# Performance work log

Hardware: AMD Instinct MI355X
Metric: run time of the kernel (lower is better)

Reference implementation:

```python
import jax, jax.numpy as jnp
import numpy as np

N_Q, N_X, N_Z = 1024, 512, 512
N_PER = N_Q + N_X + N_Z        # 2048 nodes per graph
B = 16                          # graphs per batch
DEG = 16                        # avg in/out degree
E_PER = N_PER * DEG
N = B * N_PER                   # 32768 total nodes
E = B * E_PER                   # 524288 total edges
HID, HEADS, L = 128, 4, 3
DH = HID // HEADS               # 32 per-head dim
EPS = 1e-5


def setup_inputs() -> dict:
    key = jax.random.key(0)
    ks = jax.random.split(key, 10)
    # one-hot node-type features (qubit / X-stab / Z-stab), tiled over batch
    sn = jnp.zeros((N_PER, 3), jnp.float32)
    sn = sn.at[:N_Q, 0].set(1.0).at[N_Q:N_Q + N_X, 1].set(1.0).at[N_Q + N_X:, 2].set(1.0)
    x = jnp.tile(sn, (B, 1))  # [N,3]
    # random sparse edges, graph-local then offset (mimics dense_to_sparse + Batch)
    src = jax.random.randint(ks[0], (B, E_PER), 0, N_PER)
    dst = jax.random.randint(ks[1], (B, E_PER), 0, N_PER)
    off = (jnp.arange(B) * N_PER)[:, None]
    edge_src = (src + off).reshape(-1).astype(jnp.int32)
    edge_dst = (dst + off).reshape(-1).astype(jnp.int32)
    seg = jnp.repeat(jnp.arange(B, dtype=jnp.int32), N_PER)  # graph id per node
    s = 0.05
    return dict(
        x=x, edge_src=edge_src, edge_dst=edge_dst, seg=seg,
        in_w=jax.random.normal(ks[2], (3, HID)) * s, in_b=jnp.zeros((HID,)),
        qw=jax.random.normal(ks[3], (L, HID, HID)) * s, qb=jnp.zeros((L, HID)),
        kw=jax.random.normal(ks[4], (L, HID, HID)) * s, kb=jnp.zeros((L, HID)),
        vw=jax.random.normal(ks[5], (L, HID, HID)) * s, vb=jnp.zeros((L, HID)),
        sw=jax.random.normal(ks[6], (L, HID, HID)) * s, sb=jnp.zeros((L, HID)),
        fw=jax.random.normal(ks[7], (L, HID, HID)) * s, fb=jnp.zeros((L, HID)),
        ln_g=jnp.ones((L, HID)), ln_b=jnp.zeros((L, HID)),
    )


def _layer_norm(h, g, b):
    mu = jnp.mean(h, axis=-1, keepdims=True)
    var = jnp.mean(jnp.square(h - mu), axis=-1, keepdims=True)
    return (h - mu) * jax.lax.rsqrt(var + EPS) * g + b


def reference(x, edge_src, edge_dst, seg, in_w, in_b, qw, qb, kw, kb, vw, vb,
              sw, sb, fw, fb, ln_g, ln_b):
    scale = 1.0 / jnp.sqrt(jnp.float32(DH))
    h = x @ in_w + in_b  # [N,HID]
    for i in range(L):
        h_res = h
        # TransformerConv: per-edge multi-head attention (softmax over in-neighbors)
        q = (h @ qw[i] + qb[i]).reshape(N, HEADS, DH)
        k = (h @ kw[i] + kb[i]).reshape(N, HEADS, DH)
        v = (h @ vw[i] + vb[i]).reshape(N, HEADS, DH)
        logits = jnp.einsum('ehd,ehd->eh', q[edge_dst], k[edge_src]) * scale  # [E,H]
        m = jax.ops.segment_max(logits, edge_dst, num_segments=N)             # [N,H]
        e = jnp.exp(logits - m[edge_dst])
        z = jax.ops.segment_sum(e, edge_dst, num_segments=N)                  # [N,H]
        alpha = e / z[edge_dst]
        agg = jax.ops.segment_sum(alpha[:, :, None] * v[edge_src], edge_dst,
                                  num_segments=N).reshape(N, HID)
        h = agg + h @ sw[i] + sb[i]        # root/skip linear (root_weight=True)
        # dropout is a no-op in eval mode
        h = h + jax.nn.relu(h @ fw[i] + fb[i])   # FFN residual
        h = h + h_res                            # outer residual
        h = jax.nn.relu(_layer_norm(h, ln_g[i], ln_b[i]))
    # global_mean_pool over graphs
    tot = jax.ops.segment_sum(h, seg, num_segments=B)                       # [B,HID]
    cnt = jax.ops.segment_sum(jnp.ones((N, 1), h.dtype), seg, num_segments=B)
    return tot / cnt
```

## Files before the change

### kernel.cpp

```cpp
#include <hip/hip_runtime.h>
#include <hip/hip_bf16.h>

#define N_TOT 32768
#define E_TOT 524288
#define HID 128
#define B_GR 16
#define NPER 2048
#define LAYERS 3
#define EPSLN 1e-5f
#define ELLW 64
#define SCALE_L2E (0.17677669529663687f * 1.4426950408889634f)

typedef float f4 __attribute__((ext_vector_type(4)));
typedef short bf16x8 __attribute__((ext_vector_type(8)));
typedef unsigned short u16x4 __attribute__((ext_vector_type(4)));

__device__ __forceinline__ unsigned short f2bf_rne(float x) {
    unsigned u = __float_as_uint(x);
    unsigned r = (u + 0x7FFFu + ((u >> 16) & 1u)) >> 16;
    return (unsigned short)r;
}

__device__ __forceinline__ float bf2f(unsigned short u) {
    return __uint_as_float(((unsigned)u) << 16);
}

__device__ __forceinline__ void unpack8(uint4 w, float* f) {
    f[0] = __uint_as_float(w.x << 16); f[1] = __uint_as_float(w.x & 0xFFFF0000u);
    f[2] = __uint_as_float(w.y << 16); f[3] = __uint_as_float(w.y & 0xFFFF0000u);
    f[4] = __uint_as_float(w.z << 16); f[5] = __uint_as_float(w.z & 0xFFFF0000u);
    f[6] = __uint_as_float(w.w << 16); f[7] = __uint_as_float(w.w & 0xFFFF0000u);
}

__global__ __launch_bounds__(256) void k_zp(const float* __restrict__ qw, const float* __restrict__ kw,
                                            const float* __restrict__ vw, const float* __restrict__ sw,
                                            const float* __restrict__ fw, unsigned short* __restrict__ wt,
                                            int* __restrict__ cursor, float* __restrict__ outz) {
    if (blockIdx.x < 960) {
        int mid = blockIdx.x >> 6;
        int within = (blockIdx.x & 63) * 256 + threadIdx.x;
        int l = mid / 5, t = mid % 5;
        const float* src = (t == 0 ? qw : t == 1 ? kw : t == 2 ? vw : t == 3 ? sw : fw) + l * HID * HID;
        int c = within >> 7;
        int kk = within & 127;
        int k = kk ^ ((c & 7) << 3);
        float sc = (t == 0) ? SCALE_L2E : 1.0f;
        wt[mid * HID * HID + c * HID + kk] = f2bf_rne(src[k * HID + c] * sc);
    } else if (blockIdx.x < 992) {
        int i = (blockIdx.x - 960) * 256 + threadIdx.x;
        reinterpret_cast<int4*>(cursor)[i] = int4{0, 0, 0, 0};
    } else {
        f4 z4 = {0.f, 0.f, 0.f, 0.f};
        reinterpret_cast<f4*>(outz)[threadIdx.x * 2] = z4;
        reinterpret_cast<f4*>(outz)[threadIdx.x * 2 + 1] = z4;
    }
}

#define GEMM_COMPUTE(acc, AL)                                                               \
    {                                                                                       \
        _Pragma("unroll")                                                                   \
        for (int ks = 0; ks < 4; ++ks) {                                                    \
            bf16x8 a0 = *reinterpret_cast<const bf16x8*>(                                   \
                &AL[wm * 32 + lr][(ks * 32 + lg * 8) ^ swz]);                               \
            bf16x8 a1 = *reinterpret_cast<const bf16x8*>(                                   \
                &AL[wm * 32 + 16 + lr][(ks * 32 + lg * 8) ^ swz]);                          \
            _Pragma("unroll")                                                               \
            for (int n = 0; n < 4; ++n) {                                                   \
                bf16x8 b = *reinterpret_cast<const bf16x8*>(                                \
                    &W_lds[wn * 64 + n * 16 + lr][(ks * 32 + lg * 8) ^ swz]);               \
                acc[0][n] = __builtin_amdgcn_mfma_f32_16x16x32_bf16(a0, b, acc[0][n], 0, 0, 0); \
                acc[1][n] = __builtin_amdgcn_mfma_f32_16x16x32_bf16(a1, b, acc[1][n], 0, 0, 0); \
            }                                                                               \
        }                                                                                   \
    }

#define ZERO_ACC(acc)                                                        \
    {                                                                        \
        _Pragma("unroll")                                                    \
        for (int m = 0; m < 2; ++m)                                          \
            _Pragma("unroll")                                                \
            for (int n = 0; n < 4; ++n) acc[m][n] = f4{0, 0, 0, 0};          \
    }

#define COPY_W(SRC)                                                          \
    {                                                                        \
        _Pragma("unroll")                                                    \
        for (int p = 0; p < 8; ++p)                                          \
            reinterpret_cast<uint4*>(&W_lds[0][0])[p * 256 + tid] =          \
                reinterpret_cast<const uint4*>(SRC)[p * 256 + tid];          \
    }

#define QKV_EPILOGUE(ACC, T_IDX)                                                            \
    {                                                                                       \
        _Pragma("unroll")                                                                   \
        for (int n = 0; n < 4; ++n) {                                                       \
            int col = wn * 64 + n * 16 + lr;                                                \
            float bs = biases[T_IDX][col];                                                  \
            if (T_IDX == 0) bs *= SCALE_L2E;                                                \
            unsigned short* outp = (T_IDX == 0) ? oq : okv + ((T_IDX == 2) ? 128 : 0);      \
            const size_t stride = (T_IDX == 0) ? HID : 256;                                 \
            _Pragma("unroll")                                                               \
            for (int m = 0; m < 2; ++m) {                                                   \
                _Pragma("unroll")                                                           \
                for (int r = 0; r < 4; ++r) {                                               \
                    int row = r0 + wm * 32 + m * 16 + lg * 4 + r;                           \
                    outp[(size_t)row * stride + col] = f2bf_rne(ACC[m][n][r] + bs);         \
                }                                                                           \
            }                                                                               \
        }                                                                                   \
    }

__global__ __launch_bounds__(256) void k_scatter_init(const int* __restrict__ esrc, const int* __restrict__ edst,
                                                      int* __restrict__ cursor, unsigned short* __restrict__ ell,
                                                      const float* __restrict__ x,
                                                      const float* __restrict__ in_w,
                                                      const float* __restrict__ in_b,
                                                      const unsigned short* __restrict__ wl,
                                                      const float* __restrict__ qb, const float* __restrict__ kb,
                                                      const float* __restrict__ vb,
                                                      unsigned short* __restrict__ h16,
                                                      unsigned short* __restrict__ oq,
                                                      unsigned short* __restrict__ okv) {
    __shared__ unsigned short A_lds[64][HID];
    __shared__ unsigned short W_lds[HID][HID];
    int tid = threadIdx.x;
    if (blockIdx.x < E_TOT / 256) {
        int e = blockIdx.x * 256 + tid;
        int d = edst[e];
        int pos = atomicAdd(&cursor[d], 1);
        if (pos < ELLW) ell[d * ELLW + pos] = (unsigned short)esrc[e];
        return;
    }
    int r0 = (blockIdx.x - E_TOT / 256) * 64;
    int lane = tid & 63, w = tid >> 6;
    int wm = w >> 1, wn = w & 1;
    int lr = lane & 15, lg = lane >> 4;
    int swz = (lane & 7) << 3;

    #pragma unroll
    for (int p = 0; p < 8; ++p) {
        int idx = p * 256 + tid;
        int row = idx >> 5;
        int k0 = (idx & 31) * 4;
        int n = r0 + row;
        float x0 = x[n * 3 + 0], x1 = x[n * 3 + 1], x2 = x[n * 3 + 2];
        u16x4 b;
        #pragma unroll
        for (int i = 0; i < 4; ++i) {
            int c = k0 + i;
            b[i] = f2bf_rne(x0 * in_w[c] + x1 * in_w[HID + c] + x2 * in_w[2 * HID + c] + in_b[c]);
        }
        int cs = k0 ^ ((row & 7) << 3);
        *reinterpret_cast<u16x4*>(&A_lds[row][cs]) = b;
        *reinterpret_cast<u16x4*>(&h16[(size_t)n * HID + cs]) = b;
    }

    const float* biases[3] = {qb, kb, vb};
    f4 acc[2][4];
    #pragma unroll
    for (int t = 0; t < 3; ++t) {
        COPY_W(wl + t * HID * HID);
        __syncthreads();
        ZERO_ACC(acc);
        GEMM_COMPUTE(acc, A_lds);
        QKV_EPILOGUE(acc, t);
        __syncthreads();
    }
}

__global__ __launch_bounds__(256) void k_attn5(const unsigned short* __restrict__ qb16,
                                               const unsigned short* __restrict__ kv16,
                                               const int* __restrict__ deg,
                                               const unsigned short* __restrict__ ell,
                                               unsigned short* __restrict__ outagg) {
    int bid = blockIdx.x;
    int xcd = bid & 7;
    int chunk = bid >> 3;
    int g2 = xcd + 8 * (chunk >> 9);
    int nb = g2 * 512 + (chunk & 511);
    int n = nb * 4 + (threadIdx.x >> 6);

    int lane = threadIdx.x & 63;
    int g = lane >> 4, l = lane & 15;
    int dg = deg[n];
    if (dg > ELLW) dg = ELLW;
    const unsigned short* eb = ell + n * ELLW;

    float qf[8];
    {
        uint4 qw = *reinterpret_cast<const uint4*>(&qb16[(size_t)n * HID + l * 8]);
        unpack8(qw, qf);
    }

    float z = 0.f;
    float a[8] = {0, 0, 0, 0, 0, 0, 0, 0};
    int nit = (dg + 3) >> 2;
    if (nit > 0) {
        int j = g;
        bool val = j < dg;
        int sj = val ? (int)eb[j] : 0;
        const unsigned short* kv = kv16 + (size_t)sj * 256 + l * 8;
        uint4 kw = *reinterpret_cast<const uint4*>(kv);
        uint4 vw = *reinterpret_cast<const uint4*>(kv + 128);
        for (int it = 0; it < nit; ++it) {
            int jn = j + 4;
            bool valn = jn < dg;
            int sn = valn ? (int)eb[jn] : 0;
            const unsigned short* kvn = kv16 + (size_t)sn * 256 + l * 8;
            uint4 kwn = *reinterpret_cast<const uint4*>(kvn);
            uint4 vwn = *reinterpret_cast<const uint4*>(kvn + 128);
            float kf[8]; unpack8(kw, kf);
            float d = qf[0] * kf[0] + qf[1] * kf[1] + qf[2] * kf[2] + qf[3] * kf[3] +
                      qf[4] * kf[4] + qf[5] * kf[5] + qf[6] * kf[6] + qf[7] * kf[7];
            d += __shfl_xor(d, 1);
            d += __shfl_xor(d, 2);
            float p = val ? exp2f(d) : 0.f;
            z += p;
            float vf[8]; unpack8(vw, vf);
            #pragma unroll
            for (int c = 0; c < 8; ++c) a[c] += p * vf[c];
            kw = kwn; vw = vwn; j = jn; val = valn;
        }
    }
    #pragma unroll
    for (int off = 16; off <= 32; off <<= 1) {
        z += __shfl_xor(z, off);
        #pragma unroll
        for (int c = 0; c < 8; ++c) a[c] += __shfl_xor(a[c], off);
    }
    if (g == 0) {
        float inv = (z > 0.f) ? 1.f / z : 0.f;
        uint4 o;
        o.x = (unsigned)f2bf_rne(a[0] * inv) | ((unsigned)f2bf_rne(a[1] * inv) << 16);
        o.y = (unsigned)f2bf_rne(a[2] * inv) | ((unsigned)f2bf_rne(a[3] * inv) << 16);
        o.z = (unsigned)f2bf_rne(a[4] * inv) | ((unsigned)f2bf_rne(a[5] * inv) << 16);
        o.w = (unsigned)f2bf_rne(a[6] * inv) | ((unsigned)f2bf_rne(a[7] * inv) << 16);
        *reinterpret_cast<uint4*>(&outagg[(size_t)n * HID + l * 8]) = o;
    }
}

template <bool QKV>
__global__ __launch_bounds__(256) void k_fused(const unsigned short* __restrict__ h16,
                                               const unsigned short* __restrict__ wsf,
                                               const float* __restrict__ sb,
                                               const float* __restrict__ fb,
                                               const unsigned short* __restrict__ agg16,
                                               const float* __restrict__ gma,
                                               const float* __restrict__ beta,
                                               unsigned short* __restrict__ out16,
                                               const unsigned short* __restrict__ wqkv,
                                               const float* __restrict__ qb2,
                                               const float* __restrict__ kb2,
                                               const float* __restrict__ vb2,
                                               unsigned short* __restrict__ oq,
                                               unsigned short* __restrict__ okv,
                                               float* __restrict__ pool_out) {
    __shared__ __align__(16) char smem[50432];
    unsigned short (*A_lds)[HID] = reinterpret_cast<unsigned short (*)[HID]>(smem);
    unsigned short (*W_lds)[HID] = reinterpret_cast<unsigned short (*)[HID]>(smem + 16384);
    float (*T)[133] = reinterpret_cast<float (*)[133]>(smem + 16384);

    int tid = threadIdx.x;
    int r0 = blockIdx.x * 64;
    int lane = tid & 63, w = tid >> 6;
    int wm = w >> 1, wn = w & 1;
    int lr = lane & 15, lg = lane >> 4;
    int swz = (lane & 7) << 3;

    {
        const uint4* hs = reinterpret_cast<const uint4*>(h16 + (size_t)r0 * HID);
        #pragma unroll
        for (int p = 0; p < 4; ++p)
            reinterpret_cast<uint4*>(&A_lds[0][0])[p * 256 + tid] = hs[p * 256 + tid];
    }
    COPY_W(wsf);
    __syncthreads();
    f4 acc[2][4];
    ZERO_ACC(acc);
    GEMM_COMPUTE(acc, A_lds);
    __syncthreads();

    unsigned short hres[2][4][4];
    #pragma unroll
    for (int n = 0; n < 4; ++n) {
        int col = wn * 64 + n * 16 + lr;
        float bs = sb[col];
        #pragma unroll
        for (int m = 0; m < 2; ++m) {
            #pragma unroll
            for (int r = 0; r < 4; ++r) {
                int rl = wm * 32 + m * 16 + lg * 4 + r;
                int cs = col ^ ((rl & 7) << 3);
                hres[m][n][r] = A_lds[rl][cs];
                float v = acc[m][n][r] + bs + bf2f(agg16[(size_t)(r0 + rl) * HID + col]);
                acc[m][n][r] = v;
                A_lds[rl][cs] = f2bf_rne(v);
            }
        }
    }
    COPY_W(wsf + HID * HID);
    __syncthreads();
    f4 acc2[2][4];
    ZERO_ACC(acc2);
    GEMM_COMPUTE(acc2, A_lds);
    __syncthreads();

    #pragma unroll
    for (int n = 0; n < 4; ++n) {
        int col = wn * 64 + n * 16 + lr;
        float bs = fb[col];
        #pragma unroll
        for (int m = 0; m < 2; ++m) {
            #pragma unroll
            for (int r = 0; r < 4; ++r) {
                int rl = wm * 32 + m * 16 + lg * 4 + r;
                T[rl][col] = acc[m][n][r] + fmaxf(acc2[m][n][r] + bs, 0.f) + bf2f(hres[m][n][r]);
            }
        }
    }
    __syncthreads();

    int row = tid >> 2, qd = tid & 3;
    float s = 0.f, ss = 0.f;
    #pragma unroll 8
    for (int cc = 0; cc < 32; ++cc) {
        int c = (cc + qd * 8) & 31;
        float x = T[row][qd * 32 + c];
        s += x; ss += x * x;
    }
    s += __shfl_xor(s, 1);  s += __shfl_xor(s, 2);
    ss += __shfl_xor(ss, 1); ss += __shfl_xor(ss, 2);
    float mu = s * (1.f / 128.f);
    float var = ss * (1.f / 128.f) - mu * mu;
    float rsq = rsqrtf(fmaxf(var, 0.f) + EPSLN);
    int rswz = (row & 7) << 3;
    #pragma unroll
    for (int c4 = 0; c4 < 8; ++c4) {
        int cb = ((c4 + qd * 2) & 7) * 4;
        int col = qd * 32 + cb;
        f4 o;
        #pragma unroll
        for (int i = 0; i < 4; ++i) {
            float x = T[row][col + i];
            float y = (x - mu) * rsq * gma[col + i] + beta[col + i];
            o[i] = fmaxf(y, 0.f);
        }
        if (QKV) {
            u16x4 b = {f2bf_rne(o[0]), f2bf_rne(o[1]), f2bf_rne(o[2]), f2bf_rne(o[3])};
            int cs = col ^ rswz;
            *reinterpret_cast<u16x4*>(&A_lds[row][cs]) = b;
            *reinterpret_cast<u16x4*>(&out16[(size_t)(r0 + row) * HID + cs]) = b;
        } else {
            #pragma unroll
            for (int i = 0; i < 4; ++i) T[row][col + i] = o[i];
        }
    }

    if (QKV) {
        const float* biases[3] = {qb2, kb2, vb2};
        __syncthreads();
        f4 acc3[2][4];
        #pragma unroll
        for (int t = 0; t < 3; ++t) {
            COPY_W(wqkv + t * HID * HID);
            __syncthreads();
            ZERO_ACC(acc3);
            GEMM_COMPUTE(acc3, A_lds);
            QKV_EPILOGUE(acc3, t);
            __syncthreads();
        }
    } else {
        __syncthreads();
        if (tid < HID) {
            float s2 = 0.f;
            #pragma unroll 8
            for (int r = 0; r < 64; ++r) s2 += T[r][tid];
            atomicAdd(&pool_out[(r0 >> 11) * HID + tid], s2 * (1.f / NPER));
        }
    }
}

extern "C" void kernel_launch(void* const* d_in, const int* in_sizes, int n_in,
                              void* d_out, int out_size, void* d_ws, size_t ws_size,
                              hipStream_t stream) {
    const float* x    = (const float*)d_in[0];
    const int*   esrc = (const int*)d_in[1];
    const int*   edst = (const int*)d_in[2];
    const float* in_w = (const float*)d_in[4];
    const float* in_b = (const float*)d_in[5];
    const float* qw   = (const float*)d_in[6];
    const float* qb   = (const float*)d_in[7];
    const float* kw   = (const float*)d_in[8];
    const float* kb   = (const float*)d_in[9];
    const float* vw   = (const float*)d_in[10];
    const float* vb   = (const float*)d_in[11];
    const float* sw   = (const float*)d_in[12];
    const float* sb   = (const float*)d_in[13];
    const float* fw   = (const float*)d_in[14];
    const float* fb   = (const float*)d_in[15];
    const float* ln_g = (const float*)d_in[16];
    const float* ln_b = (const float*)d_in[17];
    float* out = (float*)d_out;

    const size_t NH = (size_t)N_TOT * HID;
    unsigned short* h16   = (unsigned short*)d_ws;
    unsigned short* agg16 = h16 + NH;
    unsigned short* qb16  = agg16 + NH;
    unsigned short* kv16  = qb16 + NH;
    unsigned short* wt    = kv16 + 2 * NH;
    int* cursor = (int*)(wt + 15 * HID * HID);
    unsigned short* ell = (unsigned short*)(cursor + N_TOT);

    k_zp<<<993, 256, 0, stream>>>(qw, kw, vw, sw, fw, wt, cursor, out);
    k_scatter_init<<<E_TOT / 256 + N_TOT / 64, 256, 0, stream>>>(
        esrc, edst, cursor, ell, x, in_w, in_b, wt, qb, kb, vb, h16, qb16, kv16);

    for (int l = 0; l < LAYERS; ++l) {
        const unsigned short* wt_l = wt + (size_t)l * 5 * HID * HID;
        k_attn5<<<N_TOT / 4, 256, 0, stream>>>(qb16, kv16, cursor, ell, agg16);
        if (l + 1 < LAYERS) {
            const unsigned short* wt_n = wt + (size_t)(l + 1) * 5 * HID * HID;
            k_fused<true><<<N_TOT / 64, 256, 0, stream>>>(
                h16, wt_l + 3 * HID * HID, sb + (size_t)l * HID, fb + (size_t)l * HID,
                agg16, ln_g + (size_t)l * HID, ln_b + (size_t)l * HID, h16,
                wt_n, qb + (size_t)(l + 1) * HID, kb + (size_t)(l + 1) * HID,
                vb + (size_t)(l + 1) * HID, qb16, kv16, nullptr);
        } else {
            k_fused<false><<<N_TOT / 64, 256, 0, stream>>>(
                h16, wt_l + 3 * HID * HID, sb + (size_t)l * HID, fb + (size_t)l * HID,
                agg16, ln_g + (size_t)l * HID, ln_b + (size_t)l * HID, nullptr,
                nullptr, nullptr, nullptr, nullptr, nullptr, nullptr, out);
        }
    }
}
```

Baseline: 169.9 us.

## Read GEMM weights directly from global memory and fuse LayerNorm into registers

```diff
diff --git a/kernel.cpp b/kernel.cpp
--- a/kernel.cpp
+++ b/kernel.cpp
@@ -56,7 +56,7 @@
     }
 }
 
-#define GEMM_COMPUTE(acc, AL)                                                               \
+#define GEMM_COMPUTE_G(acc, AL, WG)                                                         \
     {                                                                                       \
         _Pragma("unroll")                                                                   \
         for (int ks = 0; ks < 4; ++ks) {                                                    \
@@ -67,7 +67,7 @@
             _Pragma("unroll")                                                               \
             for (int n = 0; n < 4; ++n) {                                                   \
                 bf16x8 b = *reinterpret_cast<const bf16x8*>(                                \
-                    &W_lds[wn * 64 + n * 16 + lr][(ks * 32 + lg * 8) ^ swz]);               \
+                    (WG) + (wn * 64 + n * 16 + lr) * HID + ((ks * 32 + lg * 8) ^ swz));     \
                 acc[0][n] = __builtin_amdgcn_mfma_f32_16x16x32_bf16(a0, b, acc[0][n], 0, 0, 0); \
                 acc[1][n] = __builtin_amdgcn_mfma_f32_16x16x32_bf16(a1, b, acc[1][n], 0, 0, 0); \
             }                                                                               \
@@ -80,14 +80,6 @@
         for (int m = 0; m < 2; ++m)                                          \
             _Pragma("unroll")                                                \
             for (int n = 0; n < 4; ++n) acc[m][n] = f4{0, 0, 0, 0};          \
-    }
-
-#define COPY_W(SRC)                                                          \
-    {                                                                        \
-        _Pragma("unroll")                                                    \
-        for (int p = 0; p < 8; ++p)                                          \
-            reinterpret_cast<uint4*>(&W_lds[0][0])[p * 256 + tid] =          \
-                reinterpret_cast<const uint4*>(SRC)[p * 256 + tid];          \
     }
 
 #define QKV_EPILOGUE(ACC, T_IDX)                                                            \
@@ -122,7 +114,6 @@
                                                       unsigned short* __restrict__ oq,
                                                       unsigned short* __restrict__ okv) {
     __shared__ unsigned short A_lds[64][HID];
-    __shared__ unsigned short W_lds[HID][HID];
     int tid = threadIdx.x;
     if (blockIdx.x < E_TOT / 256) {
         int e = blockIdx.x * 256 + tid;
@@ -154,17 +145,15 @@
         *reinterpret_cast<u16x4*>(&A_lds[row][cs]) = b;
         *reinterpret_cast<u16x4*>(&h16[(size_t)n * HID + cs]) = b;
     }
+    __syncthreads();
 
     const float* biases[3] = {qb, kb, vb};
     f4 acc[2][4];
     #pragma unroll
     for (int t = 0; t < 3; ++t) {
-        COPY_W(wl + t * HID * HID);
-        __syncthreads();
         ZERO_ACC(acc);
-        GEMM_COMPUTE(acc, A_lds);
+        GEMM_COMPUTE_G(acc, A_lds, wl + t * HID * HID);
         QKV_EPILOGUE(acc, t);
-        __syncthreads();
     }
 }
 
@@ -255,10 +244,8 @@
                                                unsigned short* __restrict__ oq,
                                                unsigned short* __restrict__ okv,
                                                float* __restrict__ pool_out) {
-    __shared__ __align__(16) char smem[50432];
-    unsigned short (*A_lds)[HID] = reinterpret_cast<unsigned short (*)[HID]>(smem);
-    unsigned short (*W_lds)[HID] = reinterpret_cast<unsigned short (*)[HID]>(smem + 16384);
-    float (*T)[133] = reinterpret_cast<float (*)[133]>(smem + 16384);
+    __shared__ unsigned short A_lds[64][HID];
+    __shared__ float RS[64][4];
 
     int tid = threadIdx.x;
     int r0 = blockIdx.x * 64;
@@ -273,11 +260,10 @@
         for (int p = 0; p < 4; ++p)
             reinterpret_cast<uint4*>(&A_lds[0][0])[p * 256 + tid] = hs[p * 256 + tid];
     }
-    COPY_W(wsf);
     __syncthreads();
     f4 acc[2][4];
     ZERO_ACC(acc);
-    GEMM_COMPUTE(acc, A_lds);
+    GEMM_COMPUTE_G(acc, A_lds, wsf);
     __syncthreads();
 
     unsigned short hres[2][4][4];
@@ -298,12 +284,10 @@
             }
         }
     }
-    COPY_W(wsf + HID * HID);
     __syncthreads();
     f4 acc2[2][4];
     ZERO_ACC(acc2);
-    GEMM_COMPUTE(acc2, A_lds);
-    __syncthreads();
+    GEMM_COMPUTE_G(acc2, A_lds, wsf + HID * HID);
 
     #pragma unroll
     for (int n = 0; n < 4; ++n) {
@@ -313,68 +297,79 @@
         for (int m = 0; m < 2; ++m) {
             #pragma unroll
             for (int r = 0; r < 4; ++r) {
+                acc[m][n][r] = acc[m][n][r] + fmaxf(acc2[m][n][r] + bs, 0.f) + bf2f(hres[m][n][r]);
+            }
+        }
+    }
+    #pragma unroll
+    for (int m = 0; m < 2; ++m) {
+        #pragma unroll
+        for (int r = 0; r < 4; ++r) {
+            float s = acc[m][0][r] + acc[m][1][r] + acc[m][2][r] + acc[m][3][r];
+            float ss = acc[m][0][r] * acc[m][0][r] + acc[m][1][r] * acc[m][1][r] +
+                       acc[m][2][r] * acc[m][2][r] + acc[m][3][r] * acc[m][3][r];
+            #pragma unroll
+            for (int off = 1; off < 16; off <<= 1) {
+                s += __shfl_xor(s, off);
+                ss += __shfl_xor(ss, off);
+            }
+            if (lr == 0) {
                 int rl = wm * 32 + m * 16 + lg * 4 + r;
-                T[rl][col] = acc[m][n][r] + fmaxf(acc2[m][n][r] + bs, 0.f) + bf2f(hres[m][n][r]);
+                RS[rl][wn * 2] = s;
+                RS[rl][wn * 2 + 1] = ss;
             }
         }
     }
     __syncthreads();
 
-    int row = tid >> 2, qd = tid & 3;
-    float s = 0.f, ss = 0.f;
-    #pragma unroll 8
-    for (int cc = 0; cc < 32; ++cc) {
-        int c = (cc + qd * 8) & 31;
-        float x = T[row][qd * 32 + c];
-        s += x; ss += x * x;
-    }
-    s += __shfl_xor(s, 1);  s += __shfl_xor(s, 2);
-    ss += __shfl_xor(ss, 1); ss += __shfl_xor(ss, 2);
-    float mu = s * (1.f / 128.f);
-    float var = ss * (1.f / 128.f) - mu * mu;
-    float rsq = rsqrtf(fmaxf(var, 0.f) + EPSLN);
-    int rswz = (row & 7) << 3;
-    #pragma unroll
-    for (int c4 = 0; c4 < 8; ++c4) {
-        int cb = ((c4 + qd * 2) & 7) * 4;
-        int col = qd * 32 + cb;
-        f4 o;
-        #pragma unroll
-        for (int i = 0; i < 4; ++i) {
-            float x = T[row][col + i];
-            float y = (x - mu) * rsq * gma[col + i] + beta[col + i];
-            o[i] = fmaxf(y, 0.f);
-        }
-        if (QKV) {
-            u16x4 b = {f2bf_rne(o[0]), f2bf_rne(o[1]), f2bf_rne(o[2]), f2bf_rne(o[3])};
-            int cs = col ^ rswz;
-            *reinterpret_cast<u16x4*>(&A_lds[row][cs]) = b;
-            *reinterpret_cast<u16x4*>(&out16[(size_t)(r0 + row) * HID + cs]) = b;
-        } else {
-            #pragma unroll
-            for (int i = 0; i < 4; ++i) T[row][col + i] = o[i];
-        }
-    }
+    float g_[4], b_[4];
+    #pragma unroll
+    for (int n = 0; n < 4; ++n) {
+        int col = wn * 64 + n * 16 + lr;
+        g_[n] = gma[col];
+        b_[n] = beta[col];
+    }
+    #pragma unroll
+    for (int m = 0; m < 2; ++m) {
+        #pragma unroll
+        for (int r = 0; r < 4; ++r) {
+            int rl = wm * 32 + m * 16 + lg * 4 + r;
+            float sum = RS[rl][0] + RS[rl][2];
+            float ssum = RS[rl][1] + RS[rl][3];
+            float mu = sum * (1.f / 128.f);
+            float var = ssum * (1.f / 128.f) - mu * mu;
+            float rsq = rsqrtf(fmaxf(var, 0.f) + EPSLN);
+            int rs = (rl & 7) << 3;
+            #pragma unroll
+            for (int n = 0; n < 4; ++n) {
+                int col = wn * 64 + n * 16 + lr;
+                float y = (acc[m][n][r] - mu) * rsq * g_[n] + b_[n];
+                A_lds[rl][col ^ rs] = f2bf_rne(fmaxf(y, 0.f));
+            }
+        }
+    }
+    __syncthreads();
 
     if (QKV) {
+        {
+            uint4* hd = reinterpret_cast<uint4*>(out16 + (size_t)r0 * HID);
+            #pragma unroll
+            for (int p = 0; p < 4; ++p)
+                hd[p * 256 + tid] = reinterpret_cast<const uint4*>(&A_lds[0][0])[p * 256 + tid];
+        }
         const float* biases[3] = {qb2, kb2, vb2};
-        __syncthreads();
         f4 acc3[2][4];
         #pragma unroll
         for (int t = 0; t < 3; ++t) {
-            COPY_W(wqkv + t * HID * HID);
-            __syncthreads();
             ZERO_ACC(acc3);
-            GEMM_COMPUTE(acc3, A_lds);
+            GEMM_COMPUTE_G(acc3, A_lds, wqkv + t * HID * HID);
             QKV_EPILOGUE(acc3, t);
-            __syncthreads();
         }
     } else {
-        __syncthreads();
         if (tid < HID) {
             float s2 = 0.f;
             #pragma unroll 8
-            for (int r = 0; r < 64; ++r) s2 += T[r][tid];
+            for (int r = 0; r < 64; ++r) s2 += bf2f(A_lds[r][tid ^ ((r & 7) << 3)]);
             atomicAdd(&pool_out[(r0 >> 11) * HID + tid], s2 * (1.f / NPER));
         }
     }
```

New measurement: 174.5 us. +2.7%, slower.

## Build ELL adjacency per graph slice in shared memory instead of global atomics

Applied to the files above, without the earlier changes.

```diff
diff --git a/kernel.cpp b/kernel.cpp
--- a/kernel.cpp
+++ b/kernel.cpp
@@ -9,6 +9,7 @@
 #define LAYERS 3
 #define EPSLN 1e-5f
 #define ELLW 64
+#define E_PER_G (E_TOT / B_GR)
 #define SCALE_L2E (0.17677669529663687f * 1.4426950408889634f)
 
 typedef float f4 __attribute__((ext_vector_type(4)));
@@ -35,7 +36,7 @@
 __global__ __launch_bounds__(256) void k_zp(const float* __restrict__ qw, const float* __restrict__ kw,
                                             const float* __restrict__ vw, const float* __restrict__ sw,
                                             const float* __restrict__ fw, unsigned short* __restrict__ wt,
-                                            int* __restrict__ cursor, float* __restrict__ outz) {
+                                            float* __restrict__ outz) {
     if (blockIdx.x < 960) {
         int mid = blockIdx.x >> 6;
         int within = (blockIdx.x & 63) * 256 + threadIdx.x;
@@ -46,9 +47,6 @@
         int k = kk ^ ((c & 7) << 3);
         float sc = (t == 0) ? SCALE_L2E : 1.0f;
         wt[mid * HID * HID + c * HID + kk] = f2bf_rne(src[k * HID + c] * sc);
-    } else if (blockIdx.x < 992) {
-        int i = (blockIdx.x - 960) * 256 + threadIdx.x;
-        reinterpret_cast<int4*>(cursor)[i] = int4{0, 0, 0, 0};
     } else {
         f4 z4 = {0.f, 0.f, 0.f, 0.f};
         reinterpret_cast<f4*>(outz)[threadIdx.x * 2] = z4;
@@ -110,28 +108,53 @@
         }                                                                                   \
     }
 
-__global__ __launch_bounds__(256) void k_scatter_init(const int* __restrict__ esrc, const int* __restrict__ edst,
-                                                      int* __restrict__ cursor, unsigned short* __restrict__ ell,
-                                                      const float* __restrict__ x,
-                                                      const float* __restrict__ in_w,
-                                                      const float* __restrict__ in_b,
-                                                      const unsigned short* __restrict__ wl,
-                                                      const float* __restrict__ qb, const float* __restrict__ kb,
-                                                      const float* __restrict__ vb,
-                                                      unsigned short* __restrict__ h16,
-                                                      unsigned short* __restrict__ oq,
-                                                      unsigned short* __restrict__ okv) {
-    __shared__ unsigned short A_lds[64][HID];
-    __shared__ unsigned short W_lds[HID][HID];
+__global__ __launch_bounds__(256) void k_ell_init(const int* __restrict__ esrc, const int* __restrict__ edst,
+                                                  int* __restrict__ deg, unsigned short* __restrict__ ell,
+                                                  const float* __restrict__ x,
+                                                  const float* __restrict__ in_w,
+                                                  const float* __restrict__ in_b,
+                                                  const unsigned short* __restrict__ wl,
+                                                  const float* __restrict__ qb, const float* __restrict__ kb,
+                                                  const float* __restrict__ vb,
+                                                  unsigned short* __restrict__ h16,
+                                                  unsigned short* __restrict__ oq,
+                                                  unsigned short* __restrict__ okv) {
+    __shared__ __align__(16) char smem[49152];
     int tid = threadIdx.x;
-    if (blockIdx.x < E_TOT / 256) {
-        int e = blockIdx.x * 256 + tid;
-        int d = edst[e];
-        int pos = atomicAdd(&cursor[d], 1);
-        if (pos < ELLW) ell[d * ELLW + pos] = (unsigned short)esrc[e];
+    if (blockIdx.x < 128) {
+        int g = blockIdx.x >> 3, q = blockIdx.x & 7;
+        int nbase = g * NPER + q * 256;
+        int* cnt = reinterpret_cast<int*>(smem);
+        unsigned short (*el)[ELLW] = reinterpret_cast<unsigned short (*)[ELLW]>(smem + 1024);
+        cnt[tid] = 0;
+        __syncthreads();
+        const int4* d4 = reinterpret_cast<const int4*>(edst + g * E_PER_G);
+        const int4* s4 = reinterpret_cast<const int4*>(esrc + g * E_PER_G);
+        for (int it = 0; it < E_PER_G / 1024; ++it) {
+            int4 dd = d4[it * 256 + tid];
+            int4 ss = s4[it * 256 + tid];
+            #pragma unroll
+            for (int j = 0; j < 4; ++j) {
+                int dv = (&dd.x)[j];
+                int sv = (&ss.x)[j];
+                unsigned local = (unsigned)(dv - nbase);
+                if (local < 256u) {
+                    int pos = atomicAdd(&cnt[local], 1);
+                    if (pos < ELLW) el[local][pos] = (unsigned short)sv;
+                }
+            }
+        }
+        __syncthreads();
+        uint4* eg = reinterpret_cast<uint4*>(ell + (size_t)nbase * ELLW);
+        const uint4* es = reinterpret_cast<const uint4*>(&el[0][0]);
+        #pragma unroll
+        for (int p = 0; p < 8; ++p) eg[p * 256 + tid] = es[p * 256 + tid];
+        deg[nbase + tid] = cnt[tid];
         return;
     }
-    int r0 = (blockIdx.x - E_TOT / 256) * 64;
+    unsigned short (*A_lds)[HID] = reinterpret_cast<unsigned short (*)[HID]>(smem);
+    unsigned short (*W_lds)[HID] = reinterpret_cast<unsigned short (*)[HID]>(smem + 16384);
+    int r0 = (blockIdx.x - 128) * 64;
     int lane = tid & 63, w = tid >> 6;
     int wm = w >> 1, wn = w & 1;
     int lr = lane & 15, lg = lane >> 4;
@@ -408,16 +431,16 @@
     unsigned short* qb16  = agg16 + NH;
     unsigned short* kv16  = qb16 + NH;
     unsigned short* wt    = kv16 + 2 * NH;
-    int* cursor = (int*)(wt + 15 * HID * HID);
-    unsigned short* ell = (unsigned short*)(cursor + N_TOT);
-
-    k_zp<<<993, 256, 0, stream>>>(qw, kw, vw, sw, fw, wt, cursor, out);
-    k_scatter_init<<<E_TOT / 256 + N_TOT / 64, 256, 0, stream>>>(
-        esrc, edst, cursor, ell, x, in_w, in_b, wt, qb, kb, vb, h16, qb16, kv16);
+    int* deg = (int*)(wt + 15 * HID * HID);
+    unsigned short* ell = (unsigned short*)(deg + N_TOT);
+
+    k_zp<<<961, 256, 0, stream>>>(qw, kw, vw, sw, fw, wt, out);
+    k_ell_init<<<128 + N_TOT / 64, 256, 0, stream>>>(
+        esrc, edst, deg, ell, x, in_w, in_b, wt, qb, kb, vb, h16, qb16, kv16);
 
     for (int l = 0; l < LAYERS; ++l) {
         const unsigned short* wt_l = wt + (size_t)l * 5 * HID * HID;
-        k_attn5<<<N_TOT / 4, 256, 0, stream>>>(qb16, kv16, cursor, ell, agg16);
+        k_attn5<<<N_TOT / 4, 256, 0, stream>>>(qb16, kv16, deg, ell, agg16);
         if (l + 1 < LAYERS) {
             const unsigned short* wt_n = wt + (size_t)(l + 1) * 5 * HID * HID;
             k_fused<true><<<N_TOT / 64, 256, 0, stream>>>(
```

Measured after the change: 156.7 us, median of 2. 1.08x faster.
